# Performance work log

Hardware: AMD Instinct MI355X
Metric: run time of the kernel (lower is better)

The kernel has to match this reference:

```python
import jax, jax.numpy as jnp
import numpy as np

EPS = 1e-6


def _normalize(A):
    # zero the diagonal, then symmetric degree normalization D @ A @ D.
    # D is diagonal with 1/(eps + sqrt(rowsum)), so D@A@D is an
    # elementwise row/column scale (same math, no NxN diag matmuls).
    N = A.shape[-1]
    A = A * (1.0 - jnp.eye(N, dtype=A.dtype))          # [B,N,N]
    d = 1.0 / (EPS + jnp.sqrt(jnp.sum(A, axis=2)))     # [B,N]
    return d[:, :, None] * A * d[:, None, :]           # [B,N,N]


def setup_inputs() -> dict:
    key = jax.random.key(0)
    k1, k2, k3, k4 = jax.random.split(key, 4)
    B, N, F, K, out_dim = 16, 2048, 64, 4, 128
    X = jax.random.uniform(k1, (B, N, F), dtype=jnp.float32)
    A = jax.random.uniform(k2, (B, N, N), dtype=jnp.float32)
    kernel = jax.random.normal(k3, (K * F, out_dim), dtype=jnp.float32) * 0.05
    bias = jax.random.normal(k4, (out_dim,), dtype=jnp.float32) * 0.05
    return {"X": X, "A": A, "kernel": kernel, "bias": bias}


def reference(X, A, kernel, bias):
    K = 4
    L = _normalize(A)                                  # [B,N,N]
    Xt = [X, jnp.matmul(L, X)]                         # T0, T1
    for k in range(2, K):
        Xt.append(2.0 * jnp.matmul(L, Xt[k - 1]) - Xt[k - 2])
    out = jnp.concatenate(Xt, axis=-1)                 # [B,N,K*F]
    out = jnp.matmul(out, kernel) + bias               # [B,N,out_dim]
    return jax.nn.relu(out)
```

## Files before the change

kernel.cpp:

```cpp
#include <hip/hip_runtime.h>

typedef __attribute__((ext_vector_type(4))) float  f32x4;
typedef __attribute__((ext_vector_type(8))) short  bf16x8;
typedef __attribute__((ext_vector_type(4))) int    i32x4;
typedef __attribute__((ext_vector_type(4))) unsigned short u16x4;

#define NB 16
#define NN 2048
#define FF 64

#define INV_SCALE (1.0f / (127.0f * 131072.0f))

__device__ __forceinline__ unsigned short f2bf(float x) {
  union { float f; unsigned int u; } c; c.f = x;
  unsigned int u = c.u;
  return (unsigned short)((u + 0x7fffu + ((u >> 16) & 1u)) >> 16);
}
__device__ __forceinline__ float bf2f(unsigned short b) {
  union { unsigned int u; float f; } c; c.u = (unsigned int)b << 16;
  return c.f;
}
__device__ __forceinline__ unsigned int fbits(float x) {
  union { float f; unsigned int u; } c; c.f = x; return c.u;
}

__device__ __forceinline__ void gload16(const void* g, void* l) {
  __builtin_amdgcn_global_load_lds(
      (const __attribute__((address_space(1))) void*)g,
      (__attribute__((address_space(3))) void*)l, 16, 0, 0);
}

#define BAR() asm volatile("s_barrier" ::: "memory")

__global__ __launch_bounds__(256) void rowsum_conv_kernel(
    const float* __restrict__ A, char* __restrict__ A8,
    float* __restrict__ dvec) {
  int row = blockIdx.x * 4 + (threadIdx.x >> 6);
  int lane = threadIdx.x & 63;
  int i = row & (NN - 1);
  const float* arow = A + (size_t)row * NN;
  char* orow = A8 + (size_t)row * NN;
  float diagval = __builtin_nontemporal_load(arow + i);
  float s = 0.f;
#pragma unroll
  for (int p = 0; p < 8; ++p) {
    int base = p * 256 + lane * 4;
    f32x4 v = __builtin_nontemporal_load((const f32x4*)(arow + base));
    s += v[0] + v[1] + v[2] + v[3];
    float y0 = fmaf(v[0], 127.f, 8388608.f);
    float y1 = fmaf(v[1], 127.f, 8388608.f);
    float y2 = fmaf(v[2], 127.f, 8388608.f);
    float y3 = fmaf(v[3], 127.f, 8388608.f);
    unsigned p01 = __builtin_amdgcn_perm(fbits(y1), fbits(y0), 0x0C0C0400u);
    unsigned p23 = __builtin_amdgcn_perm(fbits(y3), fbits(y2), 0x0C0C0400u);
    *(unsigned int*)(orow + base) =
        __builtin_amdgcn_perm(p23, p01, 0x05040100u);
  }
#pragma unroll
  for (int off = 32; off > 0; off >>= 1) s += __shfl_down(s, off, 64);
  asm volatile("s_waitcnt vmcnt(0)" ::: "memory");
  if (lane == 0) {
    orow[i] = 0;
    dvec[row] = 1.0f / (1e-6f + sqrtf(s - diagval));
  }
}

__global__ __launch_bounds__(256) void scale_transpose_kernel(
    const float* __restrict__ V, const float* __restrict__ dvec,
    char* __restrict__ Uh, char* __restrict__ Ul,
    unsigned short* __restrict__ Tb,
    const float* __restrict__ Kr, unsigned short* __restrict__ WT) {
  int bid = blockIdx.x;
  int tid = threadIdx.x;
  if (bid >= 512) {
    int idx = (bid - 512) * 256 + tid;
    int k = idx >> 7, c = idx & 127;
    WT[c * 256 + k] = f2bf(Kr[idx]);
    return;
  }
  int b = bid >> 5;
  int n0 = (bid & 31) * 64;
  __shared__ float t[64][65];
#pragma unroll
  for (int it = 0; it < 4; ++it) {
    int e = it * 256 + tid;
    int nl = e >> 4;
    int f0 = (e & 15) * 4;
    int n = n0 + nl;
    f32x4 v = *(const f32x4*)&V[((size_t)b * NN + n) * FF + f0];
    float dd = dvec[b * NN + n];
    u16x4 o;
#pragma unroll
    for (int j = 0; j < 4; ++j) { o[j] = f2bf(v[j]); t[f0 + j][nl] = v[j] * dd; }
    *(u16x4*)&Tb[((size_t)b * NN + n) * FF + f0] = o;
  }
  __syncthreads();
#pragma unroll
  for (int it = 0; it < 2; ++it) {
    int c = it * 256 + tid;
    int f = c >> 3, nl0 = (c & 7) * 8;
    unsigned long long ph = 0, pl = 0;
#pragma unroll
    for (int j = 0; j < 8; ++j) {
      int q = (int)rintf(t[f][nl0 + j] * 131072.f);
      q = q > 16383 ? 16383 : (q < -16383 ? -16383 : q);
      ph |= (unsigned long long)((unsigned int)(q >> 7) & 255u) << (8 * j);
      pl |= (unsigned long long)((unsigned int)(q & 127)) << (8 * j);
    }
    size_t o = ((size_t)b * FF + f) * NN + n0 + nl0;
    *(unsigned long long*)&Uh[o] = ph;
    *(unsigned long long*)&Ul[o] = pl;
  }
}

__global__ __launch_bounds__(512) void cheb_mm_kernel(
    const char* __restrict__ A8,
    const char* __restrict__ Uh,
    const char* __restrict__ Ul,
    const float* __restrict__ dvec,
    const unsigned short* __restrict__ prevb,
    unsigned short* __restrict__ Tbout,
    char* __restrict__ Uhout,
    char* __restrict__ Ulout,
    float cs) {
  __shared__ char lds[49152];
  int bid = blockIdx.x;
  int slot = bid >> 3;
  int b = (bid & 7) * 2 + (slot >> 5);
  int tm = slot & 31;
  int tid = threadIdx.x;
  int lane = tid & 63;
  int w = tid >> 6;
  int wm = w >> 1, wn = w & 1;
  int lr = lane >> 3;
  int gs = (lane & 7) ^ lr;
  int r16 = lane & 15, kq = lane >> 4;
  const int NT = NN / 128;

  const size_t abase = ((size_t)b * NN + (size_t)tm * 64) * NN;
  const size_t ubase = (size_t)b * FF * NN;

  i32x4 ach[2] = {};
  i32x4 acl[2] = {};

  int r = w * 8 + lr;
  auto stage = [&](int s, int kt) {
    int k0 = kt * 128;
    gload16(Uh + ubase + (size_t)r * NN + k0 + gs * 16,
            &lds[16384 + s * 8192 + w * 1024]);
    gload16(Ul + ubase + (size_t)r * NN + k0 + gs * 16,
            &lds[32768 + s * 8192 + w * 1024]);
    gload16(A8 + abase + (size_t)r * NN + k0 + gs * 16,
            &lds[s * 8192 + w * 1024]);
  };

  stage(0, 0); stage(1, 1);
  for (int t = 0; t < NT; ++t) {
    int s = t & 1;
    if (t < NT - 1) asm volatile("s_waitcnt vmcnt(3)" ::: "memory");
    else            asm volatile("s_waitcnt vmcnt(0)" ::: "memory");
    BAR();
    int ar = wm * 16 + r16;
#pragma unroll
    for (int j = 0; j < 2; ++j) {
      i32x4 af = *(const i32x4*)&lds[s * 8192 + ar * 128 +
                                     (((j * 4 + kq) ^ (ar & 7)) * 16)];
#pragma unroll
      for (int ni = 0; ni < 2; ++ni) {
        int fr = wn * 32 + ni * 16 + r16;
        int fo = fr * 128 + (((j * 4 + kq) ^ (fr & 7)) * 16);
        i32x4 uhf = *(const i32x4*)&lds[16384 + s * 8192 + fo];
        i32x4 ulf = *(const i32x4*)&lds[32768 + s * 8192 + fo];
        ach[ni] = __builtin_amdgcn_mfma_i32_16x16x64_i8(af, uhf, ach[ni], 0, 0, 0);
        acl[ni] = __builtin_amdgcn_mfma_i32_16x16x64_i8(af, ulf, acl[ni], 0, 0, 0);
      }
    }
    BAR();
    if (t + 2 < NT) stage(s, t + 2);
  }

  char (*th)[72]  = (char(*)[72])lds;
  char (*tlo)[72] = (char(*)[72])&lds[8192];
  int n0 = tm * 64;
#pragma unroll
  for (int rg = 0; rg < 4; ++rg) {
    int rl = wm * 16 + kq * 4 + rg;
    int row = n0 + rl;
    float dd = dvec[b * NN + row];
    float dcs = dd * cs;
#pragma unroll
    for (int ni = 0; ni < 2; ++ni) {
      int col = wn * 32 + ni * 16 + r16;
      size_t idx = ((size_t)b * NN + row) * FF + col;
      float c = 128.f * (float)ach[ni][rg] + (float)acl[ni][rg];
      float v = dcs * c;
      if (prevb) v -= bf2f(prevb[idx]);
      Tbout[idx] = f2bf(v);
      if (Uhout) {
        int q = (int)rintf(dd * v * 131072.f);
        q = q > 16383 ? 16383 : (q < -16383 ? -16383 : q);
        th[col][rl]  = (char)(q >> 7);
        tlo[col][rl] = (char)(q & 127);
      }
    }
  }
  if (Uhout) {
    __syncthreads();
    int f = tid >> 3, nb = (tid & 7) * 8;
    unsigned long long vh = *(const unsigned long long*)&th[f][nb];
    unsigned long long vl = *(const unsigned long long*)&tlo[f][nb];
    size_t o = ((size_t)b * FF + f) * NN + n0 + nb;
    *(unsigned long long*)&Uhout[o] = vh;
    *(unsigned long long*)&Ulout[o] = vl;
  }
}

__global__ __launch_bounds__(256) void final_gemm_kernel(
    const unsigned short* __restrict__ Tb,
    const unsigned short* __restrict__ WT,
    const float* __restrict__ bias,
    float* __restrict__ out) {
  __shared__ unsigned short lds[36864];
  const int M = NB * NN;
  int m0 = blockIdx.x * 64;
  int tid = threadIdx.x;
  int lane = tid & 63, w = tid >> 6;
  int wm = w >> 1, wn = w & 1;
  int lr = lane >> 3, gs = (lane & 7) ^ lr;
  int r16 = lane & 15, kq = lane >> 4;

  f32x4 acc[2][4] = {};

  auto stage = [&](int s, int kt) {
    const unsigned short* asrc = Tb + (size_t)kt * M * FF;
#pragma unroll
    for (int i = 0; i < 2; ++i) {
      int chunk = w * 2 + i;
      int r = chunk * 8 + lr;
      gload16(asrc + (size_t)(m0 + r) * FF + gs * 8,
              &lds[s * 4096 + chunk * 512]);
    }
#pragma unroll
    for (int i = 0; i < 4; ++i) {
      int chunk = w * 4 + i;
      int c = chunk * 8 + lr;
      gload16(WT + c * 256 + kt * 64 + gs * 8,
              &lds[12288 + s * 8192 + chunk * 512]);
    }
  };

  stage(0, 0); stage(1, 1); stage(2, 2);
  int s = 0;
  for (int t = 0; t < 4; ++t) {
    if (t < 2)       asm volatile("s_waitcnt vmcnt(12)" ::: "memory");
    else if (t == 2) asm volatile("s_waitcnt vmcnt(6)" ::: "memory");
    else             asm volatile("s_waitcnt vmcnt(0)" ::: "memory");
    BAR();
    bf16x8 af[2][2], bfr[4][2];
#pragma unroll
    for (int ks = 0; ks < 2; ++ks) {
#pragma unroll
      for (int mi = 0; mi < 2; ++mi) {
        int row = wm * 32 + mi * 16 + r16;
        af[mi][ks] = *(const bf16x8*)&lds[s * 4096 + row * 64 +
                                          (((ks * 4 + kq) ^ (row & 7)) * 8)];
      }
#pragma unroll
      for (int ni = 0; ni < 4; ++ni) {
        int fr = wn * 64 + ni * 16 + r16;
        bfr[ni][ks] = *(const bf16x8*)&lds[12288 + s * 8192 + fr * 64 +
                                           (((ks * 4 + kq) ^ (fr & 7)) * 8)];
      }
    }
#pragma unroll
    for (int ks = 0; ks < 2; ++ks)
#pragma unroll
      for (int mi = 0; mi < 2; ++mi)
#pragma unroll
        for (int ni = 0; ni < 4; ++ni)
          acc[mi][ni] = __builtin_amdgcn_mfma_f32_16x16x32_bf16(
              af[mi][ks], bfr[ni][ks], acc[mi][ni], 0, 0, 0);
    BAR();
    if (t + 3 < 4) stage(s, t + 3);
    s = (s == 2) ? 0 : s + 1;
  }

#pragma unroll
  for (int mi = 0; mi < 2; ++mi) {
#pragma unroll
    for (int r = 0; r < 4; ++r) {
      int row = m0 + wm * 32 + mi * 16 + kq * 4 + r;
#pragma unroll
      for (int ni = 0; ni < 4; ++ni) {
        int col = wn * 64 + ni * 16 + r16;
        float v = acc[mi][ni][r] + bias[col];
        out[(size_t)row * 128 + col] = v > 0.f ? v : 0.f;
      }
    }
  }
}

extern "C" void kernel_launch(void* const* d_in, const int* in_sizes, int n_in,
                              void* d_out, int out_size, void* d_ws, size_t ws_size,
                              hipStream_t stream) {
  const float* X    = (const float*)d_in[0];
  const float* A    = (const float*)d_in[1];
  const float* Kr   = (const float*)d_in[2];
  const float* bias = (const float*)d_in[3];
  float* out = (float*)d_out;
  char* ws = (char*)d_ws;

  const size_t SZ_A8 = (size_t)NB * NN * NN;
  const size_t SZ_D  = (size_t)NB * NN * 4;
  const size_t SZ_U  = (size_t)NB * FF * NN;
  const size_t SZ_TB = (size_t)NB * NN * FF * 2;
  const size_t TBE   = (size_t)NB * NN * FF;

  char*           A8  = ws;
  float*          dv  = (float*)(ws + SZ_A8);
  char*           Uha = ws + SZ_A8 + SZ_D;
  char*           Ula = Uha + SZ_U;
  char*           Uhb = Ula + SZ_U;
  char*           Ulb = Uhb + SZ_U;
  unsigned short* Tb  = (unsigned short*)(Ulb + SZ_U);
  unsigned short* WT  = (unsigned short*)(Ulb + SZ_U + 4 * SZ_TB);

  rowsum_conv_kernel<<<NB * NN / 4, 256, 0, stream>>>(A, A8, dv);
  scale_transpose_kernel<<<640, 256, 0, stream>>>(X, dv, Uha, Ula, Tb, Kr, WT);
  cheb_mm_kernel<<<512, 512, 0, stream>>>(A8, Uha, Ula, dv, nullptr,
                                          Tb + TBE, Uhb, Ulb, 1.0f * INV_SCALE);
  cheb_mm_kernel<<<512, 512, 0, stream>>>(A8, Uhb, Ulb, dv, Tb,
                                          Tb + 2 * TBE, Uha, Ula, 2.0f * INV_SCALE);
  cheb_mm_kernel<<<512, 512, 0, stream>>>(A8, Uha, Ula, dv, Tb + TBE,
                                          Tb + 3 * TBE, nullptr, nullptr, 2.0f * INV_SCALE);
  final_gemm_kernel<<<512, 256, 0, stream>>>(Tb, WT, bias, out);
}
```

Measured before the change: 117.5 us.

## Fuse final projection GEMM into the last Chebyshev matmul epilogue

Result: slower. 123.5 us (+5.1%).

```diff
diff --git a/kernel.cpp b/kernel.cpp
--- a/kernel.cpp
+++ b/kernel.cpp
@@ -8,6 +8,7 @@
 #define NB 16
 #define NN 2048
 #define FF 64
+#define TBE ((size_t)NB * NN * FF)
 
 #define INV_SCALE (1.0f / (127.0f * 131072.0f))
 
@@ -122,6 +123,10 @@
     unsigned short* __restrict__ Tbout,
     char* __restrict__ Uhout,
     char* __restrict__ Ulout,
+    const unsigned short* __restrict__ Tbz,
+    const unsigned short* __restrict__ WTg,
+    const float* __restrict__ biasg,
+    float* __restrict__ outg,
     float cs) {
   __shared__ char lds[49152];
   int bid = blockIdx.x;
@@ -179,9 +184,65 @@
     if (t + 2 < NT) stage(s, t + 2);
   }
 
+  int n0 = tm * 64;
+
+  if (WTg) {
+#pragma unroll
+    for (int tz = 0; tz < 3; ++tz) {
+      const unsigned short* src =
+          Tbz + (size_t)tz * TBE + ((size_t)b * NN + n0 + r) * FF;
+      gload16(src + gs * 8, &lds[tz * 8192 + w * 1024]);
+    }
+#pragma unroll
+    for (int rg = 0; rg < 4; ++rg) {
+      int rl = wm * 16 + kq * 4 + rg;
+      int row = n0 + rl;
+      float dcs = dvec[b * NN + row] * cs;
+#pragma unroll
+      for (int ni = 0; ni < 2; ++ni) {
+        int col = wn * 32 + ni * 16 + r16;
+        size_t idx = ((size_t)b * NN + row) * FF + col;
+        float c = 128.f * (float)ach[ni][rg] + (float)acl[ni][rg];
+        float v = dcs * c - bf2f(prevb[idx]);
+        int off = 3 * 8192 + rl * 128 + (((col >> 3) ^ (rl & 7)) * 16) +
+                  (col & 7) * 2;
+        *(unsigned short*)&lds[off] = f2bf(v);
+      }
+    }
+    asm volatile("s_waitcnt vmcnt(0)" ::: "memory");
+    __syncthreads();
+    f32x4 acc[4] = {};
+#pragma unroll
+    for (int tz = 0; tz < 4; ++tz) {
+#pragma unroll
+      for (int ks = 0; ks < 2; ++ks) {
+        int row = wm * 16 + r16;
+        bf16x8 af = *(const bf16x8*)&lds[tz * 8192 + row * 128 +
+                                         (((ks * 4 + kq) ^ (row & 7)) * 16)];
+#pragma unroll
+        for (int ni = 0; ni < 4; ++ni) {
+          int fr = wn * 64 + ni * 16 + r16;
+          bf16x8 bf = *(const bf16x8*)&WTg[fr * 256 + tz * 64 + ks * 32 + kq * 8];
+          acc[ni] = __builtin_amdgcn_mfma_f32_16x16x32_bf16(af, bf, acc[ni], 0, 0, 0);
+        }
+      }
+    }
+#pragma unroll
+    for (int ni = 0; ni < 4; ++ni) {
+      int col = wn * 64 + ni * 16 + r16;
+      float bv = biasg[col];
+#pragma unroll
+      for (int rg = 0; rg < 4; ++rg) {
+        int row = n0 + wm * 16 + kq * 4 + rg;
+        float v = acc[ni][rg] + bv;
+        outg[((size_t)b * NN + row) * 128 + col] = v > 0.f ? v : 0.f;
+      }
+    }
+    return;
+  }
+
   char (*th)[72]  = (char(*)[72])lds;
   char (*tlo)[72] = (char(*)[72])&lds[8192];
-  int n0 = tm * 64;
 #pragma unroll
   for (int rg = 0; rg < 4; ++rg) {
     int rl = wm * 16 + kq * 4 + rg;
@@ -215,91 +276,6 @@
   }
 }
 
-__global__ __launch_bounds__(256) void final_gemm_kernel(
-    const unsigned short* __restrict__ Tb,
-    const unsigned short* __restrict__ WT,
-    const float* __restrict__ bias,
-    float* __restrict__ out) {
-  __shared__ unsigned short lds[36864];
-  const int M = NB * NN;
-  int m0 = blockIdx.x * 64;
-  int tid = threadIdx.x;
-  int lane = tid & 63, w = tid >> 6;
-  int wm = w >> 1, wn = w & 1;
-  int lr = lane >> 3, gs = (lane & 7) ^ lr;
-  int r16 = lane & 15, kq = lane >> 4;
-
-  f32x4 acc[2][4] = {};
-
-  auto stage = [&](int s, int kt) {
-    const unsigned short* asrc = Tb + (size_t)kt * M * FF;
-#pragma unroll
-    for (int i = 0; i < 2; ++i) {
-      int chunk = w * 2 + i;
-      int r = chunk * 8 + lr;
-      gload16(asrc + (size_t)(m0 + r) * FF + gs * 8,
-              &lds[s * 4096 + chunk * 512]);
-    }
-#pragma unroll
-    for (int i = 0; i < 4; ++i) {
-      int chunk = w * 4 + i;
-      int c = chunk * 8 + lr;
-      gload16(WT + c * 256 + kt * 64 + gs * 8,
-              &lds[12288 + s * 8192 + chunk * 512]);
-    }
-  };
-
-  stage(0, 0); stage(1, 1); stage(2, 2);
-  int s = 0;
-  for (int t = 0; t < 4; ++t) {
-    if (t < 2)       asm volatile("s_waitcnt vmcnt(12)" ::: "memory");
-    else if (t == 2) asm volatile("s_waitcnt vmcnt(6)" ::: "memory");
-    else             asm volatile("s_waitcnt vmcnt(0)" ::: "memory");
-    BAR();
-    bf16x8 af[2][2], bfr[4][2];
-#pragma unroll
-    for (int ks = 0; ks < 2; ++ks) {
-#pragma unroll
-      for (int mi = 0; mi < 2; ++mi) {
-        int row = wm * 32 + mi * 16 + r16;
-        af[mi][ks] = *(const bf16x8*)&lds[s * 4096 + row * 64 +
-                                          (((ks * 4 + kq) ^ (row & 7)) * 8)];
-      }
-#pragma unroll
-      for (int ni = 0; ni < 4; ++ni) {
-        int fr = wn * 64 + ni * 16 + r16;
-        bfr[ni][ks] = *(const bf16x8*)&lds[12288 + s * 8192 + fr * 64 +
-                                           (((ks * 4 + kq) ^ (fr & 7)) * 8)];
-      }
-    }
-#pragma unroll
-    for (int ks = 0; ks < 2; ++ks)
-#pragma unroll
-      for (int mi = 0; mi < 2; ++mi)
-#pragma unroll
-        for (int ni = 0; ni < 4; ++ni)
-          acc[mi][ni] = __builtin_amdgcn_mfma_f32_16x16x32_bf16(
-              af[mi][ks], bfr[ni][ks], acc[mi][ni], 0, 0, 0);
-    BAR();
-    if (t + 3 < 4) stage(s, t + 3);
-    s = (s == 2) ? 0 : s + 1;
-  }
-
-#pragma unroll
-  for (int mi = 0; mi < 2; ++mi) {
-#pragma unroll
-    for (int r = 0; r < 4; ++r) {
-      int row = m0 + wm * 32 + mi * 16 + kq * 4 + r;
-#pragma unroll
-      for (int ni = 0; ni < 4; ++ni) {
-        int col = wn * 64 + ni * 16 + r16;
-        float v = acc[mi][ni][r] + bias[col];
-        out[(size_t)row * 128 + col] = v > 0.f ? v : 0.f;
-      }
-    }
-  }
-}
-
 extern "C" void kernel_launch(void* const* d_in, const int* in_sizes, int n_in,
                               void* d_out, int out_size, void* d_ws, size_t ws_size,
                               hipStream_t stream) {
@@ -314,7 +290,6 @@
   const size_t SZ_D  = (size_t)NB * NN * 4;
   const size_t SZ_U  = (size_t)NB * FF * NN;
   const size_t SZ_TB = (size_t)NB * NN * FF * 2;
-  const size_t TBE   = (size_t)NB * NN * FF;
 
   char*           A8  = ws;
   float*          dv  = (float*)(ws + SZ_A8);
@@ -328,10 +303,15 @@
   rowsum_conv_kernel<<<NB * NN / 4, 256, 0, stream>>>(A, A8, dv);
   scale_transpose_kernel<<<640, 256, 0, stream>>>(X, dv, Uha, Ula, Tb, Kr, WT);
   cheb_mm_kernel<<<512, 512, 0, stream>>>(A8, Uha, Ula, dv, nullptr,
-                                          Tb + TBE, Uhb, Ulb, 1.0f * INV_SCALE);
+                                          Tb + TBE, Uhb, Ulb,
+                                          nullptr, nullptr, nullptr, nullptr,
+                                          1.0f * INV_SCALE);
   cheb_mm_kernel<<<512, 512, 0, stream>>>(A8, Uhb, Ulb, dv, Tb,
-                                          Tb + 2 * TBE, Uha, Ula, 2.0f * INV_SCALE);
+                                          Tb + 2 * TBE, Uha, Ula,
+                                          nullptr, nullptr, nullptr, nullptr,
+                                          2.0f * INV_SCALE);
   cheb_mm_kernel<<<512, 512, 0, stream>>>(A8, Uha, Ula, dv, Tb + TBE,
-                                          Tb + 3 * TBE, nullptr, nullptr, 2.0f * INV_SCALE);
-  final_gemm_kernel<<<512, 256, 0, stream>>>(Tb, WT, bias, out);
-}
+                                          nullptr, nullptr, nullptr,
+                                          Tb, WT, bias, out,
+                                          2.0f * INV_SCALE);
+}
```
